# Performance work log

Measured on AMD Instinct MI355X. Metric: run time of the kernel, lower is better.

## Reference

```python
import jax, jax.numpy as jnp
import numpy as np

N = 100000   # nodes
R = 8        # relations
E = 800000   # edges per relation
D = 128      # in_feat == out_feat
B = 4        # num bases
L = 2        # ngnn layers


def setup_inputs() -> dict:
    key = jax.random.key(0)
    ks = jax.random.split(key, 8)
    x = jax.random.normal(ks[0], (N, D), dtype=jnp.float32)
    edge_src = jax.random.randint(ks[1], (R, E), 0, N, dtype=jnp.int64)
    edge_dst = jax.random.randint(ks[2], (R, E), 0, N, dtype=jnp.int64)
    scale = 1.0 / np.sqrt(D)
    w_comp = jax.random.normal(ks[3], (R, B), dtype=jnp.float32) * 0.3
    bases = jax.random.normal(ks[4], (B, D, D), dtype=jnp.float32) * scale
    loop_weight = jax.random.normal(ks[5], (D, D), dtype=jnp.float32) * scale
    h_bias = jnp.zeros((D,), dtype=jnp.float32)
    ngnn_w = jax.random.normal(ks[6], (L, D, D), dtype=jnp.float32) * scale
    return {"x": x, "edge_src": edge_src, "edge_dst": edge_dst,
            "w_comp": w_comp, "bases": bases, "loop_weight": loop_weight,
            "h_bias": h_bias, "ngnn_w": ngnn_w}


def reference(x, edge_src, edge_dst, w_comp, bases, loop_weight, h_bias, ngnn_w):
    # basis-decomposed per-relation weights: [R, D, D]
    weight = jnp.einsum('rb,bio->rio', w_comp, bases)
    h = jnp.zeros((N, D), dtype=x.dtype)
    # per-relation GraphConv, norm='right' (mean over in-degree, clamp min 1),
    # in_feat == out_feat so DGL aggregates first then applies weight;
    # HeteroGraphConv sums relation outputs for the shared dst type.
    for r in range(R):
        src, dst = edge_src[r], edge_dst[r]
        msg = jax.ops.segment_sum(x[src], dst, num_segments=N)           # [N, D]
        deg = jax.ops.segment_sum(jnp.ones((E,), x.dtype), dst, num_segments=N)
        agg = msg / jnp.maximum(deg, 1.0)[:, None]
        h = h + agg @ weight[r]
    # self loop + bias + activation
    h = jax.nn.relu(h + x @ loop_weight + h_bias)
    # NGNN MLP (dropout is identity in eval)
    for l in range(ngnn_w.shape[0]):
        h = jax.nn.relu(h @ ngnn_w[l])
    return h
```

## Files before the change

kernel.cpp:

```cpp
#include <hip/hip_runtime.h>
#include <hip/hip_bf16.h>

#define N_NODES 100000
#define R_REL   8
#define E_EDGES 800000
#define D_FEAT  128
#define B_BASES 4
#define RN      (R_REL * N_NODES)
#define RE      (R_REL * E_EDGES)

#define NBKT    784
#define BKT_CAP 9216
#define P1_TPB  256
#define P1_EPT  32
#define P1_CHUNK (P1_TPB * P1_EPT)
#define P1_NWG  ((RE + P1_CHUNK - 1) / P1_CHUNK)

typedef __attribute__((ext_vector_type(8))) short short8;
typedef __attribute__((ext_vector_type(4))) float floatx4;

__global__ __launch_bounds__(1024) void init_cursor_kernel(int* __restrict__ gcursor) {
    int t = threadIdx.x;
    if (t < NBKT) gcursor[t] = t * BKT_CAP;
}

__global__ __launch_bounds__(256) void xcvt_kernel(
    const float* __restrict__ x, uint* __restrict__ xb) {
    int i = blockIdx.x * 256 + threadIdx.x;
    if (i >= N_NODES * 64) return;
    float2 v = *(const float2*)(x + 2 * (size_t)i);
    __hip_bfloat162 h = __float22bfloat162_rn(v);
    xb[i] = *(uint*)&h;
}

__global__ __launch_bounds__(256) void wcvt_kernel(
    const float* __restrict__ bases, const float* __restrict__ loopw,
    unsigned short* __restrict__ wT) {
    int idx = blockIdx.x * 256 + threadIdx.x;
    if (idx >= 128 * 640) return;
    int n = idx / 640, k = idx % 640;
    float v = (k < 512) ? bases[(size_t)k * 128 + n] : loopw[(size_t)(k - 512) * 128 + n];
    __hip_bfloat16 h = __float2bfloat16(v);
    wT[idx] = *(unsigned short*)&h;
}

__global__ __launch_bounds__(256) void wcvt2_kernel(
    const float* __restrict__ ngnn_w, unsigned short* __restrict__ wT2) {
    int idx = blockIdx.x * 256 + threadIdx.x;
    if (idx >= 2 * 128 * 128) return;
    int l = idx >> 14, rem = idx & 16383;
    int n = rem >> 7, k = rem & 127;
    float v = ngnn_w[(size_t)l * 16384 + (size_t)k * 128 + n];
    __hip_bfloat16 h = __float2bfloat16(v);
    wT2[idx] = *(unsigned short*)&h;
}

__global__ __launch_bounds__(256) void p1_kernel(
    const int* __restrict__ src, const int* __restrict__ dst,
    int* __restrict__ gcursor, int* __restrict__ ebuf2) {
    __shared__ int hist[NBKT];
    __shared__ int cnt2[NBKT];
    __shared__ int basebkt[NBKT];
    __shared__ int lofs[NBKT];
    __shared__ int aux[256];
    __shared__ int recs[P1_CHUNK];
    __shared__ unsigned short bb[P1_CHUNK];
    int t = threadIdx.x;
    for (int i = t; i < NBKT; i += 256) { hist[i] = 0; cnt2[i] = 0; }
    __syncthreads();

    int e0 = blockIdx.x * P1_CHUNK;
    int rec[P1_EPT];
    int bkt[P1_EPT];
#pragma unroll
    for (int i = 0; i < P1_EPT; ++i) {
        int e = e0 + i * P1_TPB + t;
        if (e < RE) {
            int d = dst[e];
            int s = src[e];
            int r = e / E_EDGES;
            bkt[i] = d >> 7;
            rec[i] = s | ((d & 127) << 17) | (r << 24);
            atomicAdd(&hist[bkt[i]], 1);
        } else bkt[i] = -1;
    }
    __syncthreads();

    int k0 = t * 4;
    int c0 = (k0 + 0 < NBKT) ? hist[k0 + 0] : 0;
    int c1 = (k0 + 1 < NBKT) ? hist[k0 + 1] : 0;
    int c2 = (k0 + 2 < NBKT) ? hist[k0 + 2] : 0;
    int c3 = (k0 + 3 < NBKT) ? hist[k0 + 3] : 0;
    int s1 = c0 + c1, s2 = s1 + c2, s3 = s2 + c3;
    aux[t] = s3;
    __syncthreads();
    int vv = s3;
    for (int off = 1; off < 256; off <<= 1) {
        int yv = (t >= off) ? aux[t - off] : 0;
        __syncthreads();
        vv += yv;
        aux[t] = vv;
        __syncthreads();
    }
    int total = aux[255];
    int texcl = vv - s3;
    if (k0 + 0 < NBKT) lofs[k0 + 0] = texcl;
    if (k0 + 1 < NBKT) lofs[k0 + 1] = texcl + c0;
    if (k0 + 2 < NBKT) lofs[k0 + 2] = texcl + s1;
    if (k0 + 3 < NBKT) lofs[k0 + 3] = texcl + s2;
    __syncthreads();
    for (int i = t; i < NBKT; i += 256) {
        int hv = hist[i];
        basebkt[i] = (hv > 0) ? atomicAdd(&gcursor[i], hv) : 0;
    }
    __syncthreads();

#pragma unroll
    for (int i = 0; i < P1_EPT; ++i) {
        if (bkt[i] >= 0) {
            int p = lofs[bkt[i]] + atomicAdd(&cnt2[bkt[i]], 1);
            recs[p] = rec[i];
            bb[p] = (unsigned short)bkt[i];
        }
    }
    __syncthreads();

    for (int i = t; i < total; i += 256) {
        int b = bb[i];
        int p2 = basebkt[b] + (i - lofs[b]);
        if (p2 < (b + 1) * BKT_CAP) ebuf2[p2] = recs[i];
    }
}

template <bool XB>
__global__ __launch_bounds__(1024, 8) void agg2_kernel(
    const float* __restrict__ x,
    const uint*  __restrict__ xb,
    const int*   __restrict__ gcursor,
    const int*   __restrict__ ebuf2,
    const float* __restrict__ w_comp,
    __hip_bfloat162* __restrict__ y) {
    __shared__ int raw[BKT_CAP];
    __shared__ int sorted[BKT_CAP];
    __shared__ int cursors[1024];
    __shared__ int segbeg[1024];
    const int t = threadIdx.x;
    const int bucket = blockIdx.x;

    int cnt = gcursor[bucket] - bucket * BKT_CAP;
    if (cnt > BKT_CAP) cnt = BKT_CAP;
    const int* brec = ebuf2 + (size_t)bucket * BKT_CAP;
    for (int i = t; i < cnt; i += 1024) raw[i] = brec[i];
    cursors[t] = 0;
    __syncthreads();

    for (int i = t; i < cnt; i += 1024) {
        int rec = raw[i];
        int key = ((rec >> 17) & 127) * 8 + ((rec >> 24) & 7);
        atomicAdd(&cursors[key], 1);
    }
    __syncthreads();

    int deg = cursors[t];
    int* aux = sorted;
    aux[t] = deg;
    __syncthreads();
    int vv = deg;
    for (int off = 1; off < 1024; off <<= 1) {
        int yv = (t >= off) ? aux[t - off] : 0;
        __syncthreads();
        vv += yv;
        aux[t] = vv;
        __syncthreads();
    }
    int beg = vv - deg;
    cursors[t] = beg;
    segbeg[t]  = beg;
    __syncthreads();

    for (int i = t; i < cnt; i += 1024) {
        int rec = raw[i];
        int key = ((rec >> 17) & 127) * 8 + ((rec >> 24) & 7);
        int pos = atomicAdd(&cursors[key], 1);
        sorted[pos] = rec & 0x1FFFF;
    }
    __syncthreads();

    const int wid = t >> 6, lane = t & 63;
    const float* xp  = x + 2 * lane;
    const uint*  xbp = xb + lane;
    for (int nn = 0; nn < 8; ++nn) {
        int nl = wid * 8 + nn;
        int node = bucket * 128 + nl;
        int key0 = nl * 8;
        float2 acc[B_BASES];
#pragma unroll
        for (int b = 0; b < B_BASES; ++b) acc[b] = make_float2(0.f, 0.f);
#pragma unroll
        for (int r = 0; r < R_REL; ++r) {
            int b0 = segbeg[key0 + r];
            int e0 = cursors[key0 + r];
            int d = e0 - b0;
            float inv = 1.0f / (float)(d > 1 ? d : 1);
            float ax = 0.f, ay = 0.f;
            int i = b0;
            for (; i + 3 < e0; i += 4) {
                int s0 = sorted[i], s1 = sorted[i + 1], s2 = sorted[i + 2], s3 = sorted[i + 3];
                if (XB) {
                    uint u0 = xbp[(size_t)s0 * 64];
                    uint u1 = xbp[(size_t)s1 * 64];
                    uint u2 = xbp[(size_t)s2 * 64];
                    uint u3 = xbp[(size_t)s3 * 64];
                    ax += (__uint_as_float(u0 << 16) + __uint_as_float(u1 << 16))
                        + (__uint_as_float(u2 << 16) + __uint_as_float(u3 << 16));
                    ay += (__uint_as_float(u0 & 0xFFFF0000u) + __uint_as_float(u1 & 0xFFFF0000u))
                        + (__uint_as_float(u2 & 0xFFFF0000u) + __uint_as_float(u3 & 0xFFFF0000u));
                } else {
                    float2 a = *(const float2*)(xp + (size_t)s0 * D_FEAT);
                    float2 b = *(const float2*)(xp + (size_t)s1 * D_FEAT);
                    float2 cc = *(const float2*)(xp + (size_t)s2 * D_FEAT);
                    float2 d2 = *(const float2*)(xp + (size_t)s3 * D_FEAT);
                    ax += (a.x + b.x) + (cc.x + d2.x);
                    ay += (a.y + b.y) + (cc.y + d2.y);
                }
            }
            for (; i < e0; ++i) {
                int s = sorted[i];
                if (XB) {
                    uint u = xbp[(size_t)s * 64];
                    ax += __uint_as_float(u << 16);
                    ay += __uint_as_float(u & 0xFFFF0000u);
                } else {
                    float2 a = *(const float2*)(xp + (size_t)s * D_FEAT);
                    ax += a.x; ay += a.y;
                }
            }
#pragma unroll
            for (int b = 0; b < B_BASES; ++b) {
                float coef = w_comp[r * B_BASES + b] * inv;
                acc[b].x = fmaf(coef, ax, acc[b].x);
                acc[b].y = fmaf(coef, ay, acc[b].y);
            }
        }
        if (node < N_NODES) {
#pragma unroll
            for (int b = 0; b < B_BASES; ++b)
                y[(size_t)node * 256 + b * 64 + lane] = __float22bfloat162_rn(acc[b]);
        }
    }
}

__global__ __launch_bounds__(256) void gemm_big_mfma(
    const short* __restrict__ y,
    const float* __restrict__ x,
    const unsigned short* __restrict__ wT,
    const float* __restrict__ bias,
    unsigned short* __restrict__ hb1) {
    const int wave = threadIdx.x >> 6;
    const int lane = threadIdx.x & 63;
    const int quad = lane >> 4;
    const int l16  = lane & 15;
    const int row0 = blockIdx.x * 64 + wave * 16;
    int arow = row0 + l16;
    if (arow >= N_NODES) arow = N_NODES - 1;

    floatx4 acc[8];
#pragma unroll
    for (int nt = 0; nt < 8; ++nt) acc[nt] = (floatx4){0.f, 0.f, 0.f, 0.f};

    const short* yrow = y + (size_t)arow * 512;
    const float* xrow = x + (size_t)arow * 128;
    const int koff = quad * 8;

    for (int ks = 0; ks < 16; ++ks) {
        int k0 = ks * 32 + koff;
        short8 a = *(const short8*)(yrow + k0);
#pragma unroll
        for (int nt = 0; nt < 8; ++nt) {
            int n = nt * 16 + l16;
            short8 b = *(const short8*)((const short*)wT + (size_t)n * 640 + k0);
            acc[nt] = __builtin_amdgcn_mfma_f32_16x16x32_bf16(a, b, acc[nt], 0, 0, 0);
        }
    }
#pragma unroll
    for (int ks = 0; ks < 4; ++ks) {
        int k0 = ks * 32 + koff;
        float4 fa = *(const float4*)(xrow + k0);
        float4 fb = *(const float4*)(xrow + k0 + 4);
        union { short8 s; uint u[4]; } ua;
        __hip_bfloat162 h0 = __float22bfloat162_rn(make_float2(fa.x, fa.y));
        __hip_bfloat162 h1 = __float22bfloat162_rn(make_float2(fa.z, fa.w));
        __hip_bfloat162 h2 = __float22bfloat162_rn(make_float2(fb.x, fb.y));
        __hip_bfloat162 h3 = __float22bfloat162_rn(make_float2(fb.z, fb.w));
        ua.u[0] = *(uint*)&h0; ua.u[1] = *(uint*)&h1;
        ua.u[2] = *(uint*)&h2; ua.u[3] = *(uint*)&h3;
#pragma unroll
        for (int nt = 0; nt < 8; ++nt) {
            int n = nt * 16 + l16;
            short8 b = *(const short8*)((const short*)wT + (size_t)n * 640 + 512 + k0);
            acc[nt] = __builtin_amdgcn_mfma_f32_16x16x32_bf16(ua.s, b, acc[nt], 0, 0, 0);
        }
    }

#pragma unroll
    for (int nt = 0; nt < 8; ++nt) {
        int n = nt * 16 + l16;
        float bs = bias[n];
#pragma unroll
        for (int i = 0; i < 4; ++i) {
            int m = row0 + quad * 4 + i;
            if (m < N_NODES) {
                float v = fmaxf(acc[nt][i] + bs, 0.f);
                __hip_bfloat16 h = __float2bfloat16(v);
                hb1[(size_t)m * D_FEAT + n] = *(unsigned short*)&h;
            }
        }
    }
}

template <bool OUT_BF16>
__global__ __launch_bounds__(256) void ngnn_mfma(
    const short* __restrict__ A,
    const unsigned short* __restrict__ wTl,
    void* __restrict__ C) {
    const int wave = threadIdx.x >> 6;
    const int lane = threadIdx.x & 63;
    const int quad = lane >> 4;
    const int l16  = lane & 15;
    const int row0 = blockIdx.x * 64 + wave * 16;
    int arow = row0 + l16;
    if (arow >= N_NODES) arow = N_NODES - 1;

    floatx4 acc[8];
#pragma unroll
    for (int nt = 0; nt < 8; ++nt) acc[nt] = (floatx4){0.f, 0.f, 0.f, 0.f};

    const short* ar = A + (size_t)arow * 128;
    const int koff = quad * 8;
#pragma unroll
    for (int ks = 0; ks < 4; ++ks) {
        int k0 = ks * 32 + koff;
        short8 a = *(const short8*)(ar + k0);
#pragma unroll
        for (int nt = 0; nt < 8; ++nt) {
            int n = nt * 16 + l16;
            short8 b = *(const short8*)((const short*)wTl + (size_t)n * 128 + k0);
            acc[nt] = __builtin_amdgcn_mfma_f32_16x16x32_bf16(a, b, acc[nt], 0, 0, 0);
        }
    }

#pragma unroll
    for (int nt = 0; nt < 8; ++nt) {
        int n = nt * 16 + l16;
#pragma unroll
        for (int i = 0; i < 4; ++i) {
            int m = row0 + quad * 4 + i;
            if (m < N_NODES) {
                float v = fmaxf(acc[nt][i], 0.f);
                if (OUT_BF16) {
                    __hip_bfloat16 h = __float2bfloat16(v);
                    ((unsigned short*)C)[(size_t)m * D_FEAT + n] = *(unsigned short*)&h;
                } else {
                    ((float*)C)[(size_t)m * D_FEAT + n] = v;
                }
            }
        }
    }
}

extern "C" void kernel_launch(void* const* d_in, const int* in_sizes, int n_in,
                              void* d_out, int out_size, void* d_ws, size_t ws_size,
                              hipStream_t stream) {
    const float* x           = (const float*)d_in[0];
    const int*   edge_src    = (const int*)d_in[1];
    const int*   edge_dst    = (const int*)d_in[2];
    const float* w_comp      = (const float*)d_in[3];
    const float* bases       = (const float*)d_in[4];
    const float* loop_weight = (const float*)d_in[5];
    const float* h_bias      = (const float*)d_in[6];
    const float* ngnn_w      = (const float*)d_in[7];
    float* out = (float*)d_out;

    char* ws = (char*)d_ws;
    size_t off = 0;
    __hip_bfloat162* y = (__hip_bfloat162*)(ws + off);
    off += (size_t)N_NODES * 512 * 2;
    int* ebuf2 = (int*)(ws + off);
    unsigned short* hb1 = (unsigned short*)(ws + off);
    off += (size_t)NBKT * BKT_CAP * 4;
    int* gcursor = (int*)(ws + off);
    off += 4096;
    unsigned short* wT = (unsigned short*)(ws + off);
    off += (size_t)128 * 640 * 2;
    unsigned short* wT2 = (unsigned short*)(ws + off);
    off += (size_t)2 * 128 * 128 * 2;
    uint* xb = (uint*)(ws + off);
    size_t xb_bytes = (size_t)N_NODES * 64 * 4;
    const bool use_bf16_x = (ws_size >= off + xb_bytes);
    unsigned short* hb2 = use_bf16_x ? (unsigned short*)xb : (unsigned short*)y;

    const int GEMM_GRID = (N_NODES + 63) / 64;

    wcvt_kernel<<<(128 * 640 + 255) / 256, 256, 0, stream>>>(bases, loop_weight, wT);
    wcvt2_kernel<<<(2 * 128 * 128 + 255) / 256, 256, 0, stream>>>(ngnn_w, wT2);
    if (use_bf16_x)
        xcvt_kernel<<<(N_NODES * 64 + 255) / 256, 256, 0, stream>>>(x, xb);

    init_cursor_kernel<<<1, 1024, 0, stream>>>(gcursor);
    p1_kernel<<<P1_NWG, P1_TPB, 0, stream>>>(edge_src, edge_dst, gcursor, ebuf2);

    if (use_bf16_x)
        agg2_kernel<true><<<NBKT, 1024, 0, stream>>>(x, xb, gcursor, ebuf2, w_comp, y);
    else
        agg2_kernel<false><<<NBKT, 1024, 0, stream>>>(x, nullptr, gcursor, ebuf2, w_comp, y);

    gemm_big_mfma<<<GEMM_GRID, 256, 0, stream>>>(
        (const short*)y, x, wT, h_bias, hb1);

    ngnn_mfma<true><<<GEMM_GRID, 256, 0, stream>>>(
        (const short*)hb1, wT2, (void*)hb2);
    ngnn_mfma<false><<<GEMM_GRID, 256, 0, stream>>>(
        (const short*)hb2, wT2 + 128 * 128, (void*)out);
}
```

Before: 705.7 us.

## Split each aggregation bucket across four sub-workgroups with ballot compaction

The aggregation kernel now launches four 512-thread workgroups per bucket. Each one scans the whole bucket's edge records and uses wave ballot and popcount to keep only the records whose destination falls in its 32-node slice. It then counting-sorts that smaller subset in shared memory and aggregates 4 nodes per wave. The aim is more workgroups, smaller LDS footprint and better occupancy and latency hiding. The cost is that every record in a bucket is read from global memory four times, and a slice is truncated if it exceeds the sub-capacity.

```diff
diff --git a/kernel.cpp b/kernel.cpp
--- a/kernel.cpp
+++ b/kernel.cpp
@@ -15,6 +15,10 @@
 #define P1_EPT  32
 #define P1_CHUNK (P1_TPB * P1_EPT)
 #define P1_NWG  ((RE + P1_CHUNK - 1) / P1_CHUNK)
+
+#define SUB_PER_BKT 4
+#define SGRID   (NBKT * SUB_PER_BKT)
+#define SUBCAP  2816
 
 typedef __attribute__((ext_vector_type(8))) short short8;
 typedef __attribute__((ext_vector_type(4))) float floatx4;
@@ -133,65 +137,84 @@
 }
 
 template <bool XB>
-__global__ __launch_bounds__(1024, 8) void agg2_kernel(
+__global__ __launch_bounds__(512, 8) void agg3_kernel(
     const float* __restrict__ x,
     const uint*  __restrict__ xb,
     const int*   __restrict__ gcursor,
     const int*   __restrict__ ebuf2,
     const float* __restrict__ w_comp,
     __hip_bfloat162* __restrict__ y) {
-    __shared__ int raw[BKT_CAP];
-    __shared__ int sorted[BKT_CAP];
-    __shared__ int cursors[1024];
-    __shared__ int segbeg[1024];
+    __shared__ int raw[SUBCAP];
+    __shared__ int sorted[SUBCAP];
+    __shared__ int cursors[256];
+    __shared__ int segbeg[256];
+    __shared__ int nraw;
     const int t = threadIdx.x;
-    const int bucket = blockIdx.x;
+    const int bucket = blockIdx.x % NBKT;
+    const int sub    = blockIdx.x / NBKT;
 
     int cnt = gcursor[bucket] - bucket * BKT_CAP;
     if (cnt > BKT_CAP) cnt = BKT_CAP;
     const int* brec = ebuf2 + (size_t)bucket * BKT_CAP;
-    for (int i = t; i < cnt; i += 1024) raw[i] = brec[i];
-    cursors[t] = 0;
-    __syncthreads();
-
-    for (int i = t; i < cnt; i += 1024) {
-        int rec = raw[i];
-        int key = ((rec >> 17) & 127) * 8 + ((rec >> 24) & 7);
-        atomicAdd(&cursors[key], 1);
-    }
-    __syncthreads();
-
-    int deg = cursors[t];
+    if (t < 256) cursors[t] = 0;
+    if (t == 0) nraw = 0;
+    __syncthreads();
+
+    const int lane = t & 63;
+    const unsigned long long lmask = (1ull << lane) - 1ull;
+
+    for (int i0 = 0; i0 < cnt; i0 += 512) {
+        int i = i0 + t;
+        int rec = (i < cnt) ? brec[i] : 0;
+        bool match = (i < cnt) && ((((rec >> 17) & 127) >> 5) == sub);
+        unsigned long long mask = __ballot(match);
+        int base = 0;
+        if (lane == 0) base = atomicAdd(&nraw, (int)__popcll(mask));
+        base = __shfl(base, 0);
+        if (match) {
+            int p = base + (int)__popcll(mask & lmask);
+            if (p < SUBCAP) {
+                raw[p] = rec;
+                int key = ((rec >> 17) & 31) * 8 + ((rec >> 24) & 7);
+                atomicAdd(&cursors[key], 1);
+            }
+        }
+    }
+    __syncthreads();
+    int n = nraw; if (n > SUBCAP) n = SUBCAP;
+
+    int deg = (t < 256) ? cursors[t] : 0;
     int* aux = sorted;
     aux[t] = deg;
     __syncthreads();
     int vv = deg;
-    for (int off = 1; off < 1024; off <<= 1) {
-        int yv = (t >= off) ? aux[t - off] : 0;
+    for (int off = 1; off < 256; off <<= 1) {
+        int yv = (t >= off && t < 256) ? aux[t - off] : 0;
         __syncthreads();
         vv += yv;
         aux[t] = vv;
         __syncthreads();
     }
-    int beg = vv - deg;
-    cursors[t] = beg;
-    segbeg[t]  = beg;
-    __syncthreads();
-
-    for (int i = t; i < cnt; i += 1024) {
+    if (t < 256) {
+        cursors[t] = vv - deg;
+        segbeg[t]  = vv - deg;
+    }
+    __syncthreads();
+
+    for (int i = t; i < n; i += 512) {
         int rec = raw[i];
-        int key = ((rec >> 17) & 127) * 8 + ((rec >> 24) & 7);
+        int key = ((rec >> 17) & 31) * 8 + ((rec >> 24) & 7);
         int pos = atomicAdd(&cursors[key], 1);
         sorted[pos] = rec & 0x1FFFF;
     }
     __syncthreads();
 
-    const int wid = t >> 6, lane = t & 63;
+    const int wid = t >> 6;
     const float* xp  = x + 2 * lane;
     const uint*  xbp = xb + lane;
-    for (int nn = 0; nn < 8; ++nn) {
-        int nl = wid * 8 + nn;
-        int node = bucket * 128 + nl;
+    for (int nn = 0; nn < 4; ++nn) {
+        int nl = wid * 4 + nn;
+        int node = bucket * 128 + sub * 32 + nl;
         int key0 = nl * 8;
         float2 acc[B_BASES];
 #pragma unroll
@@ -410,9 +433,9 @@
     p1_kernel<<<P1_NWG, P1_TPB, 0, stream>>>(edge_src, edge_dst, gcursor, ebuf2);
 
     if (use_bf16_x)
-        agg2_kernel<true><<<NBKT, 1024, 0, stream>>>(x, xb, gcursor, ebuf2, w_comp, y);
+        agg3_kernel<true><<<SGRID, 512, 0, stream>>>(x, xb, gcursor, ebuf2, w_comp, y);
     else
-        agg2_kernel<false><<<NBKT, 1024, 0, stream>>>(x, nullptr, gcursor, ebuf2, w_comp, y);
+        agg3_kernel<false><<<SGRID, 512, 0, stream>>>(x, nullptr, gcursor, ebuf2, w_comp, y);
 
     gemm_big_mfma<<<GEMM_GRID, 256, 0, stream>>>(
         (const short*)y, x, wT, h_bias, hb1);
```

After: 701.2 us. No clear change (-0.6%).
